# Kernel optimization log

Hardware: AMD Instinct MI355X
Metric: run time of the kernel (lower is better)

## Reference

```python
import jax, jax.numpy as jnp
import numpy as np

V, B, C, H, W, D, G = 5, 1, 32, 384, 384, 4, 8


def _rot(a, b, c):
    ca, sa = np.cos(a), np.sin(a)
    cb, sb = np.cos(b), np.sin(b)
    cc, sc = np.cos(c), np.sin(c)
    Rx = np.array([[1, 0, 0], [0, ca, -sa], [0, sa, ca]])
    Ry = np.array([[cb, 0, sb], [0, 1, 0], [-sb, 0, cb]])
    Rz = np.array([[cc, -sc, 0], [sc, cc, 0], [0, 0, 1]])
    return (Rz @ Ry @ Rx).astype(np.float32)


def setup_inputs():
    key = jax.random.key(0)
    ks = jax.random.split(key, 8)
    features = jax.random.normal(ks[0], (V, B, C, H, W), jnp.float32)
    current_depths = jax.random.uniform(ks[1], (B, D, H, W), jnp.float32, 425.0, 935.0)
    rng = np.random.RandomState(0)
    Ks = np.zeros((B, V, 3, 3), np.float32)
    Es = np.zeros((B, V, 3, 4), np.float32)
    for b in range(B):
        for v in range(V):
            f = 0.8 * W * (1.0 + 0.01 * rng.randn())
            Ks[b, v] = np.array([[f, 0, W / 2.0], [0, f, H / 2.0], [0, 0, 1.0]], np.float32)
            if v == 0:
                Rm = np.eye(3, dtype=np.float32)
                t = np.zeros(3, np.float32)
            else:
                Rm = _rot(*(0.02 * rng.randn(3)))
                t = np.array([25.0 * v, 5.0 * rng.randn(), 5.0 * rng.randn()], np.float32)
            Es[b, v, :, :3] = Rm
            Es[b, v, :, 3] = t
    w0 = 0.3 * jax.random.normal(ks[2], (16, G), jnp.float32)
    b0 = jnp.zeros((16,), jnp.float32)
    w1 = 0.3 * jax.random.normal(ks[3], (8, 16), jnp.float32)
    b1 = jnp.zeros((8,), jnp.float32)
    w2 = 0.3 * jax.random.normal(ks[4], (1, 8), jnp.float32)
    b2 = jnp.zeros((1,), jnp.float32)
    return {"features": features, "current_depths": current_depths,
            "cam_intrinsic": jnp.asarray(Ks), "cam_extrinsic": jnp.asarray(Es),
            "w0": w0, "b0": b0, "w1": w1, "b1": b1, "w2": w2, "b2": b2}


def _bilinear_sample(feat, px, py):
    # feat [B,C,H,W]; px,py [B,N] pixel coords (align_corners=True), zero padding
    Bn, Cn, Hn, Wn = feat.shape
    ff = feat.reshape(Bn, Cn, Hn * Wn)
    x0 = jnp.floor(px)
    y0 = jnp.floor(py)
    wx1 = px - x0
    wx0 = 1.0 - wx1
    wy1 = py - y0
    wy0 = 1.0 - wy1

    def gather(xi, yi, w):
        valid = (xi >= 0) & (xi <= Wn - 1) & (yi >= 0) & (yi <= Hn - 1)
        xc = jnp.clip(xi, 0, Wn - 1).astype(jnp.int32)
        yc = jnp.clip(yi, 0, Hn - 1).astype(jnp.int32)
        idx = yc * Wn + xc  # [B,N]
        v = jnp.take_along_axis(ff, idx[:, None, :], axis=2)  # [B,C,N]
        return v * (w * valid)[:, None, :]

    return (gather(x0, y0, wx0 * wy0) + gather(x0 + 1.0, y0, wx1 * wy0)
            + gather(x0, y0 + 1.0, wx0 * wy1) + gather(x0 + 1.0, y0 + 1.0, wx1 * wy1))


def _pixelwise_net(sim, w0, b0, w1, b1, w2, b2):
    # PixelwiseNet: 1x1x1 Conv3d G->16->8->1 (BN folded to identity, eval stats), sigmoid, max over depth
    x = jax.nn.relu(jnp.einsum('og,bgdhw->bodhw', w0, sim) + b0[None, :, None, None, None])
    x = jax.nn.relu(jnp.einsum('oc,bcdhw->bodhw', w1, x) + b1[None, :, None, None, None])
    x = jnp.einsum('oc,bcdhw->bodhw', w2, x) + b2[None, :, None, None, None]
    return jnp.max(jax.nn.sigmoid(x), axis=2)  # [B,1,H,W]


def reference(features, current_depths, cam_intrinsic, cam_extrinsic, w0, b0, w1, b1, w2, b2):
    ref_feat = features[0]                                   # [B,C,H,W]
    ref_g = ref_feat.reshape(B, G, C // G, H, W)
    # pixel grid with half-pixel centers, homogeneous [3, H*W]
    xs = jnp.arange(W, dtype=jnp.float32) + 0.5
    ys = jnp.arange(H, dtype=jnp.float32) + 0.5
    gx, gy = jnp.meshgrid(xs, ys)                            # [H,W]
    grid = jnp.stack([gx.ravel(), gy.ravel(), jnp.ones(H * W, jnp.float32)], 0)
    K_ref_inv = jnp.linalg.inv(cam_intrinsic[:, 0])          # [B,3,3]
    R = cam_extrinsic[:, :, :3, :3]                          # [B,V,3,3]
    t = cam_extrinsic[:, :, :3, 3:4]                         # [B,V,3,1]
    R_ref_inv = jnp.linalg.inv(R[:, 0])                      # [B,3,3]
    uv = jnp.einsum('bij,jn->bin', K_ref_inv, grid)          # [B,3,HW]
    cam_pts = uv[:, None] * current_depths.reshape(B, D, 1, H * W)   # [B,D,3,HW]
    world = jnp.einsum('bij,bdjn->bdin', R_ref_inv, cam_pts - t[:, 0:1])
    world = world.transpose(0, 2, 1, 3).reshape(B, 3, D * H * W)     # [B,3,N], N=D*H*W
    sim_sum = 0.0
    w_sum = 0.0
    for s in range(1, V):
        cp = jnp.einsum('bij,bjn->bin', R[:, s], world) + t[:, s]    # [B,3,N]
        uvd = jnp.einsum('bij,bjn->bin', cam_intrinsic[:, s], cp)
        z = uvd[:, 2] + 1e-9
        px = uvd[:, 0] / z
        py = uvd[:, 1] / z
        warped = _bilinear_sample(features[s], px, py)               # [B,C,N]
        warped = warped.reshape(B, G, C // G, D, H, W)
        sim = jnp.mean(warped * ref_g[:, :, :, None], axis=2)        # [B,G,D,H,W]
        vw = _pixelwise_net(sim, w0, b0, w1, b1, w2, b2)             # [B,1,H,W]
        sim_sum = sim_sum + sim * vw[:, :, None]
        w_sum = w_sum + vw[:, :, None]
    return sim_sum / w_sum
```

## Files before the change

### kernel.cpp

```cpp
#include <hip/hip_runtime.h>
#include <math.h>

#define Vn 5
#define Cn 32
#define Hn 384
#define Wn 384
#define Dn 4
#define Gn 8
#define HWn (Hn*Wn)

__device__ __forceinline__ void inv3(const float* m, float* o){
    float a=m[0],b=m[1],c=m[2],d=m[3],e=m[4],f=m[5],g=m[6],h=m[7],i=m[8];
    float A =  e*i - f*h;
    float B = -(d*i - f*g);
    float C =  d*h - e*g;
    float det = a*A + b*B + c*C;
    float r = 1.f/det;
    o[0] = A*r;            o[1] = -(b*i - c*h)*r;  o[2] =  (b*f - c*e)*r;
    o[3] = B*r;            o[4] =  (a*i - c*g)*r;  o[5] = -(a*f - c*d)*r;
    o[6] = C*r;            o[7] = -(a*h - b*g)*r;  o[8] =  (a*e - b*d)*r;
}
__device__ __forceinline__ void mm3(const float* a, const float* b, float* o){
    #pragma unroll
    for (int r=0;r<3;r++)
        #pragma unroll
        for (int c=0;c<3;c++)
            o[r*3+c] = a[r*3+0]*b[0*3+c] + a[r*3+1]*b[1*3+c] + a[r*3+2]*b[2*3+c];
}
__device__ __forceinline__ void mv3(const float* a, const float* v, float* o){
    #pragma unroll
    for (int r=0;r<3;r++)
        o[r] = a[r*3+0]*v[0] + a[r*3+1]*v[1] + a[r*3+2]*v[2];
}

__device__ __forceinline__ unsigned short f2bf(float f){
    unsigned int x = __float_as_uint(f);
    unsigned int r = (x + 0x7fffu + ((x >> 16) & 1u)) >> 16;
    return (unsigned short)r;
}

__global__ __launch_bounds__(256)
void transpose_kernel(const float* __restrict__ feat, unsigned short* __restrict__ featT){
    __shared__ float tile[32][257];
    const int s  = blockIdx.y;
    const int p0 = blockIdx.x * 256;
    const int t  = threadIdx.x;
    const float* src = feat + (size_t)(s+1)*Cn*HWn + p0;
    #pragma unroll
    for (int k=0;k<8;k++){
        const int i   = k*256 + t;
        const int px4 = (i & 63) * 4;
        const int ch  = i >> 6;
        const float4 v = *(const float4*)(src + (size_t)ch*HWn + px4);
        tile[ch][px4+0]=v.x; tile[ch][px4+1]=v.y; tile[ch][px4+2]=v.z; tile[ch][px4+3]=v.w;
    }
    __syncthreads();
    uint4* dst = (uint4*)(featT + ((size_t)s*HWn + p0 + t)*Cn);
    #pragma unroll
    for (int q=0;q<4;q++){
        uint4 o;
        o.x = (unsigned int)f2bf(tile[8*q+0][t]) | ((unsigned int)f2bf(tile[8*q+1][t]) << 16);
        o.y = (unsigned int)f2bf(tile[8*q+2][t]) | ((unsigned int)f2bf(tile[8*q+3][t]) << 16);
        o.z = (unsigned int)f2bf(tile[8*q+4][t]) | ((unsigned int)f2bf(tile[8*q+5][t]) << 16);
        o.w = (unsigned int)f2bf(tile[8*q+6][t]) | ((unsigned int)f2bf(tile[8*q+7][t]) << 16);
        dst[q] = o;
    }
}

#define CONSUME_PAIR(u0, u1, g)                                            \
    {                                                                      \
        const float d0 = __uint_as_float((u0) << 16);                      \
        const float d1 = __uint_as_float((u0) & 0xffff0000u);              \
        const float d2 = __uint_as_float((u1) << 16);                      \
        const float d3 = __uint_as_float((u1) & 0xffff0000u);              \
        float dt = d0*ref[(g)*4+0];                                        \
        dt = fmaf(d1, ref[(g)*4+1], dt);                                   \
        dt = fmaf(d2, ref[(g)*4+2], dt);                                   \
        dt = fmaf(d3, ref[(g)*4+3], dt);                                   \
        sg[(g)] = fmaf(w, dt, sg[(g)]);                                    \
    }

__device__ __forceinline__ void tap_bf16(const unsigned short* __restrict__ vbase,
                                         int xc, int yc, float w,
                                         const float* ref, float* sg)
{
    if (w != 0.f){
        const uint4* p = (const uint4*)(vbase + ((size_t)yc*Wn + xc)*Cn);
        const uint4 q0 = p[0];
        const uint4 q1 = p[1];
        const uint4 q2 = p[2];
        const uint4 q3 = p[3];
        CONSUME_PAIR(q0.x, q0.y, 0)
        CONSUME_PAIR(q0.z, q0.w, 1)
        CONSUME_PAIR(q1.x, q1.y, 2)
        CONSUME_PAIR(q1.z, q1.w, 3)
        CONSUME_PAIR(q2.x, q2.y, 4)
        CONSUME_PAIR(q2.z, q2.w, 5)
        CONSUME_PAIR(q3.x, q3.y, 6)
        CONSUME_PAIR(q3.z, q3.w, 7)
    }
}

__global__ __launch_bounds__(256, 2)
void gbinet_kernel(const float* __restrict__ feat,
                   const float* __restrict__ depths,
                   const float* __restrict__ Kin,
                   const float* __restrict__ Ein,
                   const float* __restrict__ w0, const float* __restrict__ b0,
                   const float* __restrict__ w1, const float* __restrict__ b1,
                   const float* __restrict__ w2, const float* __restrict__ b2,
                   const unsigned short* __restrict__ featT,
                   float* __restrict__ out)
{
    __shared__ float sW0[128], sW1[128], sB0[16], sB1[8], sW2[8], sB2s[1];
    __shared__ float sM[48];
    __shared__ float sRef[64*33];
    __shared__ float sDep[4*65];
    __shared__ float sOut[64*33];
    const int t = threadIdx.x;
    if (t < 128){ sW0[t] = w0[t]; sW1[t] = w1[t]; }
    if (t < 16) sB0[t] = b0[t];
    if (t < 8){ sB1[t] = b1[t]; sW2[t] = w2[t]; }

    const int blockBase = blockIdx.x * 64;
    {
        const float* srcR = feat + blockBase;
        #pragma unroll
        for (int k=0;k<8;k++){
            const int i  = k*256 + t;
            const int c  = i >> 6;
            const int px = i & 63;
            sRef[px*33 + c] = srcR[(size_t)c*HWn + px];
        }
        const int dp = t >> 6;
        const int px = t & 63;
        sDep[dp*65 + px] = depths[(size_t)dp*HWn + blockBase + px];
    }

    if (t == 0){
        sB2s[0] = b2[0];
        float K0inv[9]; inv3(Kin, K0inv);
        float R0[9], t0[3];
        #pragma unroll
        for (int r=0;r<3;r++){
            #pragma unroll
            for (int c=0;c<3;c++) R0[r*3+c] = Ein[r*4+c];
            t0[r] = Ein[r*4+3];
        }
        float R0inv[9]; inv3(R0, R0inv);
        float M0[9]; mm3(R0inv, K0inv, M0);
        float Rt0[3]; mv3(R0inv, t0, Rt0);
        for (int s=1;s<Vn;s++){
            const float* Ks = Kin + s*9;
            const float* Es = Ein + s*12;
            float Rs[9], ts[3];
            #pragma unroll
            for (int r=0;r<3;r++){
                #pragma unroll
                for (int c=0;c<3;c++) Rs[r*3+c] = Es[r*4+c];
                ts[r] = Es[r*4+3];
            }
            float T1[9]; mm3(Rs, M0, T1);
            float A[9];  mm3(Ks, T1, A);
            float Rr[3]; mv3(Rs, Rt0, Rr);
            float tv[3] = { ts[0]-Rr[0], ts[1]-Rr[1], ts[2]-Rr[2] };
            float cv[3]; mv3(Ks, tv, cv);
            float* dm = &sM[(s-1)*12];
            #pragma unroll
            for (int i=0;i<9;i++) dm[i] = A[i];
            #pragma unroll
            for (int i=0;i<3;i++) dm[9+i] = cv[i];
        }
    }
    __syncthreads();

    const int pixLocal = t >> 2;
    const int s        = t & 3;
    const int pix      = blockBase + pixLocal;
    const float xg = (float)(pix % Wn) + 0.5f;
    const float yg = (float)(pix / Wn) + 0.5f;

    float ref[Cn];
    #pragma unroll
    for (int c=0;c<Cn;c++) ref[c] = sRef[pixLocal*33 + c];
    float dep[Dn];
    #pragma unroll
    for (int d=0;d<Dn;d++) dep[d] = sDep[d*65 + pixLocal];

    const float* M = &sM[s*12];
    const float bx = M[0]*xg + M[1]*yg + M[2];
    const float by = M[3]*xg + M[4]*yg + M[5];
    const float bz = M[6]*xg + M[7]*yg + M[8];
    const float cx = M[9], cy = M[10], cz = M[11];
    const unsigned short* vbase = featT + (size_t)s*HWn*Cn;

    float sim[Gn][Dn];
    #pragma unroll
    for (int d=0;d<Dn;d++){
        const float dd = dep[d];
        const float ux = fmaf(bx, dd, cx);
        const float uy = fmaf(by, dd, cy);
        const float uz = fmaf(bz, dd, cz) + 1e-9f;
        const float rz = 1.f/uz;
        const float px = ux*rz, py = uy*rz;
        const float x0 = floorf(px), y0 = floorf(py);
        const float wx1 = px - x0, wy1 = py - y0;
        const float wx0 = 1.f - wx1, wy0 = 1.f - wy1;
        const bool vx0 = (x0 >= 0.f)     && (x0 <= (float)(Wn-1));
        const bool vx1 = (x0 >= -1.f)    && (x0 <= (float)(Wn-2));
        const bool vy0 = (y0 >= 0.f)     && (y0 <= (float)(Hn-1));
        const bool vy1 = (y0 >= -1.f)    && (y0 <= (float)(Hn-2));
        const float w00 = (vx0&&vy0) ? wx0*wy0 : 0.f;
        const float w10 = (vx1&&vy0) ? wx1*wy0 : 0.f;
        const float w01 = (vx0&&vy1) ? wx0*wy1 : 0.f;
        const float w11 = (vx1&&vy1) ? wx1*wy1 : 0.f;
        const int xi0 = (int)fminf(fmaxf(x0,     0.f), (float)(Wn-1));
        const int xi1 = (int)fminf(fmaxf(x0+1.f, 0.f), (float)(Wn-1));
        const int yi0 = (int)fminf(fmaxf(y0,     0.f), (float)(Hn-1));
        const int yi1 = (int)fminf(fmaxf(y0+1.f, 0.f), (float)(Hn-1));

        float sg[Gn];
        #pragma unroll
        for (int g=0; g<Gn; g++) sg[g] = 0.f;
        tap_bf16(vbase, xi0, yi0, w00, ref, sg);
        tap_bf16(vbase, xi1, yi0, w10, ref, sg);
        tap_bf16(vbase, xi0, yi1, w01, ref, sg);
        tap_bf16(vbase, xi1, yi1, w11, ref, sg);
        #pragma unroll
        for (int g=0; g<Gn; g++) sim[g][d] = sg[g]*0.25f;
    }

    float maxlog = -3.0e38f;
    #pragma unroll
    for (int d=0; d<Dn; d++){
        float h[16];
        #pragma unroll
        for (int o=0;o<16;o++){
            float a = sB0[o];
            #pragma unroll
            for (int g=0; g<Gn; g++) a = fmaf(sW0[o*Gn+g], sim[g][d], a);
            h[o] = fmaxf(a, 0.f);
        }
        float lg = sB2s[0];
        #pragma unroll
        for (int o=0;o<8;o++){
            float a = sB1[o];
            #pragma unroll
            for (int i=0;i<16;i++) a = fmaf(sW1[o*16+i], h[i], a);
            lg = fmaf(sW2[o], fmaxf(a, 0.f), lg);
        }
        maxlog = fmaxf(maxlog, lg);
    }
    const float vw = 1.f/(1.f + __expf(-maxlog));

    float wsum = vw;
    wsum += __shfl_xor(wsum, 1);
    wsum += __shfl_xor(wsum, 2);
    #pragma unroll
    for (int g=0;g<Gn;g++)
        #pragma unroll
        for (int d=0;d<Dn;d++){
            float v = sim[g][d]*vw;
            v += __shfl_xor(v, 1);
            v += __shfl_xor(v, 2);
            sim[g][d] = v;
        }

    if (s == 0){
        const float invw = 1.f/wsum;
        #pragma unroll
        for (int g=0;g<Gn;g++)
            #pragma unroll
            for (int d=0;d<Dn;d++)
                sOut[pixLocal*33 + g*Dn + d] = sim[g][d]*invw;
    }
    __syncthreads();

    float* oBase = out + blockBase;
    #pragma unroll
    for (int k=0;k<8;k++){
        const int e     = k*256 + t;
        const int plane = e >> 6;
        const int pixel = e & 63;
        oBase[(size_t)plane*HWn + pixel] = sOut[pixel*33 + plane];
    }
}

extern "C" void kernel_launch(void* const* d_in, const int* in_sizes, int n_in,
                              void* d_out, int out_size, void* d_ws, size_t ws_size,
                              hipStream_t stream)
{
    (void)in_sizes; (void)n_in; (void)out_size; (void)ws_size;
    const float* feat   = (const float*)d_in[0];
    const float* depths = (const float*)d_in[1];
    const float* K      = (const float*)d_in[2];
    const float* E      = (const float*)d_in[3];
    const float* w0     = (const float*)d_in[4];
    const float* b0     = (const float*)d_in[5];
    const float* w1     = (const float*)d_in[6];
    const float* b1     = (const float*)d_in[7];
    const float* w2     = (const float*)d_in[8];
    const float* b2     = (const float*)d_in[9];
    float* out = (float*)d_out;
    unsigned short* featT = (unsigned short*)d_ws;

    dim3 g(HWn/256, Vn-1);
    transpose_kernel<<<g, 256, 0, stream>>>(feat, featT);
    gbinet_kernel<<<HWn/64, 256, 0, stream>>>(feat, depths, K, E,
                                              w0,b0,w1,b1,w2,b2, featT, out);
}
```

Measured before the change: 253.8 us.

## Store warped features as fp16 and use packed fdot2 for similarity dot products

The transposed feature copy now stores fp16 instead of bf16, and the per-tap channel dot products use the packed v_dot2 fp16 instruction with fp32 accumulation. This replaces the shift/mask unpacking and four scalar FMAs per group. The 0.25 mean factor is folded into the bilinear weights, and the pixelwise MLP now handles two depths per pass so each shared-memory weight load is reused. fp16 has less range than bf16, which could overflow for large feature values, and the precision of the result changes.

```diff
diff --git a/kernel.cpp b/kernel.cpp
--- a/kernel.cpp
+++ b/kernel.cpp
@@ -8,6 +8,16 @@
 #define Dn 4
 #define Gn 8
 #define HWn (Hn*Wn)
+
+typedef _Float16 h2 __attribute__((ext_vector_type(2)));
+
+__device__ __forceinline__ float fdot2h(h2 a, h2 b, float c){
+#if __has_builtin(__builtin_amdgcn_fdot2)
+    return __builtin_amdgcn_fdot2(a, b, c, false);
+#else
+    return (float)a.x*(float)b.x + (float)a.y*(float)b.y + c;
+#endif
+}
 
 __device__ __forceinline__ void inv3(const float* m, float* o){
     float a=m[0],b=m[1],c=m[2],d=m[3],e=m[4],f=m[5],g=m[6],h=m[7],i=m[8];
@@ -33,10 +43,11 @@
         o[r] = a[r*3+0]*v[0] + a[r*3+1]*v[1] + a[r*3+2]*v[2];
 }
 
-__device__ __forceinline__ unsigned short f2bf(float f){
-    unsigned int x = __float_as_uint(f);
-    unsigned int r = (x + 0x7fffu + ((x >> 16) & 1u)) >> 16;
-    return (unsigned short)r;
+__device__ __forceinline__ unsigned int packh2(float a, float b){
+    h2 h;
+    h.x = (_Float16)a;
+    h.y = (_Float16)b;
+    return __builtin_bit_cast(unsigned int, h);
 }
 
 __global__ __launch_bounds__(256)
@@ -59,30 +70,25 @@
     #pragma unroll
     for (int q=0;q<4;q++){
         uint4 o;
-        o.x = (unsigned int)f2bf(tile[8*q+0][t]) | ((unsigned int)f2bf(tile[8*q+1][t]) << 16);
-        o.y = (unsigned int)f2bf(tile[8*q+2][t]) | ((unsigned int)f2bf(tile[8*q+3][t]) << 16);
-        o.z = (unsigned int)f2bf(tile[8*q+4][t]) | ((unsigned int)f2bf(tile[8*q+5][t]) << 16);
-        o.w = (unsigned int)f2bf(tile[8*q+6][t]) | ((unsigned int)f2bf(tile[8*q+7][t]) << 16);
+        o.x = packh2(tile[8*q+0][t], tile[8*q+1][t]);
+        o.y = packh2(tile[8*q+2][t], tile[8*q+3][t]);
+        o.z = packh2(tile[8*q+4][t], tile[8*q+5][t]);
+        o.w = packh2(tile[8*q+6][t], tile[8*q+7][t]);
         dst[q] = o;
     }
 }
 
-#define CONSUME_PAIR(u0, u1, g)                                            \
-    {                                                                      \
-        const float d0 = __uint_as_float((u0) << 16);                      \
-        const float d1 = __uint_as_float((u0) & 0xffff0000u);              \
-        const float d2 = __uint_as_float((u1) << 16);                      \
-        const float d3 = __uint_as_float((u1) & 0xffff0000u);              \
-        float dt = d0*ref[(g)*4+0];                                        \
-        dt = fmaf(d1, ref[(g)*4+1], dt);                                   \
-        dt = fmaf(d2, ref[(g)*4+2], dt);                                   \
-        dt = fmaf(d3, ref[(g)*4+3], dt);                                   \
-        sg[(g)] = fmaf(w, dt, sg[(g)]);                                    \
-    }
-
-__device__ __forceinline__ void tap_bf16(const unsigned short* __restrict__ vbase,
-                                         int xc, int yc, float w,
-                                         const float* ref, float* sg)
+#define DOTG(uA, uB, g)                                                        \
+    {                                                                          \
+        const h2 pa = __builtin_bit_cast(h2, (uA));                            \
+        const h2 pb = __builtin_bit_cast(h2, (uB));                            \
+        const float dt = fdot2h(pa, r2[2*(g)], fdot2h(pb, r2[2*(g)+1], 0.f));  \
+        sg[(g)] = fmaf(w, dt, sg[(g)]);                                        \
+    }
+
+__device__ __forceinline__ void tap_f16(const unsigned short* __restrict__ vbase,
+                                        int xc, int yc, float w,
+                                        const h2* r2, float* sg)
 {
     if (w != 0.f){
         const uint4* p = (const uint4*)(vbase + ((size_t)yc*Wn + xc)*Cn);
@@ -90,14 +96,14 @@
         const uint4 q1 = p[1];
         const uint4 q2 = p[2];
         const uint4 q3 = p[3];
-        CONSUME_PAIR(q0.x, q0.y, 0)
-        CONSUME_PAIR(q0.z, q0.w, 1)
-        CONSUME_PAIR(q1.x, q1.y, 2)
-        CONSUME_PAIR(q1.z, q1.w, 3)
-        CONSUME_PAIR(q2.x, q2.y, 4)
-        CONSUME_PAIR(q2.z, q2.w, 5)
-        CONSUME_PAIR(q3.x, q3.y, 6)
-        CONSUME_PAIR(q3.z, q3.w, 7)
+        DOTG(q0.x, q0.y, 0)
+        DOTG(q0.z, q0.w, 1)
+        DOTG(q1.x, q1.y, 2)
+        DOTG(q1.z, q1.w, 3)
+        DOTG(q2.x, q2.y, 4)
+        DOTG(q2.z, q2.w, 5)
+        DOTG(q3.x, q3.y, 6)
+        DOTG(q3.z, q3.w, 7)
     }
 }
 
@@ -180,9 +186,12 @@
     const float xg = (float)(pix % Wn) + 0.5f;
     const float yg = (float)(pix / Wn) + 0.5f;
 
-    float ref[Cn];
-    #pragma unroll
-    for (int c=0;c<Cn;c++) ref[c] = sRef[pixLocal*33 + c];
+    h2 r2[16];
+    #pragma unroll
+    for (int k=0;k<16;k++){
+        r2[k].x = (_Float16)sRef[pixLocal*33 + 2*k];
+        r2[k].y = (_Float16)sRef[pixLocal*33 + 2*k+1];
+    }
     float dep[Dn];
     #pragma unroll
     for (int d=0;d<Dn;d++) dep[d] = sDep[d*65 + pixLocal];
@@ -210,10 +219,10 @@
         const bool vx1 = (x0 >= -1.f)    && (x0 <= (float)(Wn-2));
         const bool vy0 = (y0 >= 0.f)     && (y0 <= (float)(Hn-1));
         const bool vy1 = (y0 >= -1.f)    && (y0 <= (float)(Hn-2));
-        const float w00 = (vx0&&vy0) ? wx0*wy0 : 0.f;
-        const float w10 = (vx1&&vy0) ? wx1*wy0 : 0.f;
-        const float w01 = (vx0&&vy1) ? wx0*wy1 : 0.f;
-        const float w11 = (vx1&&vy1) ? wx1*wy1 : 0.f;
+        const float w00 = (vx0&&vy0) ? 0.25f*wx0*wy0 : 0.f;
+        const float w10 = (vx1&&vy0) ? 0.25f*wx1*wy0 : 0.f;
+        const float w01 = (vx0&&vy1) ? 0.25f*wx0*wy1 : 0.f;
+        const float w11 = (vx1&&vy1) ? 0.25f*wx1*wy1 : 0.f;
         const int xi0 = (int)fminf(fmaxf(x0,     0.f), (float)(Wn-1));
         const int xi1 = (int)fminf(fmaxf(x0+1.f, 0.f), (float)(Wn-1));
         const int yi0 = (int)fminf(fmaxf(y0,     0.f), (float)(Hn-1));
@@ -222,34 +231,46 @@
         float sg[Gn];
         #pragma unroll
         for (int g=0; g<Gn; g++) sg[g] = 0.f;
-        tap_bf16(vbase, xi0, yi0, w00, ref, sg);
-        tap_bf16(vbase, xi1, yi0, w10, ref, sg);
-        tap_bf16(vbase, xi0, yi1, w01, ref, sg);
-        tap_bf16(vbase, xi1, yi1, w11, ref, sg);
-        #pragma unroll
-        for (int g=0; g<Gn; g++) sim[g][d] = sg[g]*0.25f;
+        tap_f16(vbase, xi0, yi0, w00, r2, sg);
+        tap_f16(vbase, xi1, yi0, w10, r2, sg);
+        tap_f16(vbase, xi0, yi1, w01, r2, sg);
+        tap_f16(vbase, xi1, yi1, w11, r2, sg);
+        #pragma unroll
+        for (int g=0; g<Gn; g++) sim[g][d] = sg[g];
     }
 
     float maxlog = -3.0e38f;
     #pragma unroll
-    for (int d=0; d<Dn; d++){
-        float h[16];
+    for (int dp=0; dp<2; dp++){
+        const int d0 = 2*dp, d1 = 2*dp+1;
+        float hx[16], hy[16];
         #pragma unroll
         for (int o=0;o<16;o++){
-            float a = sB0[o];
-            #pragma unroll
-            for (int g=0; g<Gn; g++) a = fmaf(sW0[o*Gn+g], sim[g][d], a);
-            h[o] = fmaxf(a, 0.f);
-        }
-        float lg = sB2s[0];
+            float ax = sB0[o], ay = sB0[o];
+            #pragma unroll
+            for (int g=0; g<Gn; g++){
+                const float wv = sW0[o*Gn+g];
+                ax = fmaf(wv, sim[g][d0], ax);
+                ay = fmaf(wv, sim[g][d1], ay);
+            }
+            hx[o] = fmaxf(ax, 0.f);
+            hy[o] = fmaxf(ay, 0.f);
+        }
+        float lgx = sB2s[0], lgy = sB2s[0];
         #pragma unroll
         for (int o=0;o<8;o++){
-            float a = sB1[o];
-            #pragma unroll
-            for (int i=0;i<16;i++) a = fmaf(sW1[o*16+i], h[i], a);
-            lg = fmaf(sW2[o], fmaxf(a, 0.f), lg);
-        }
-        maxlog = fmaxf(maxlog, lg);
+            float ax = sB1[o], ay = sB1[o];
+            #pragma unroll
+            for (int i=0;i<16;i++){
+                const float wv = sW1[o*16+i];
+                ax = fmaf(wv, hx[i], ax);
+                ay = fmaf(wv, hy[i], ay);
+            }
+            const float w2v = sW2[o];
+            lgx = fmaf(w2v, fmaxf(ax, 0.f), lgx);
+            lgy = fmaf(w2v, fmaxf(ay, 0.f), lgy);
+        }
+        maxlog = fmaxf(maxlog, fmaxf(lgx, lgy));
     }
     const float vw = 1.f/(1.f + __expf(-maxlog));
 
```

Result: faster. 242.3 us (-4.5%).
